# Performance work log

Hardware: AMD Instinct MI355X
Metric: run time of the kernel (lower is better)

The kernel has to match this reference:

```python
import jax, jax.numpy as jnp
import numpy as np
from functools import partial

INPUT_DIM = 256
HIDDEN = 512
NUM_LAYERS = 2

def _linp(key, fan_in, shape):
    # torch nn.Linear/Conv default init: U(-1/sqrt(fan_in), 1/sqrt(fan_in))
    bound = 1.0 / np.sqrt(fan_in)
    return jax.random.uniform(key, shape, jnp.float32, -bound, bound)

def setup_inputs() -> dict:
    key = jax.random.key(0)
    ks = iter(jax.random.split(key, 64))
    d = {}
    d["x"] = jax.random.normal(next(ks), (32, 16, 1, 64, 64), jnp.float32)
    # encoder convs (OIHW)
    d["conv1_w"] = _linp(next(ks), 1 * 9, (16, 1, 3, 3));   d["conv1_b"] = _linp(next(ks), 1 * 9, (16,))
    d["conv2_w"] = _linp(next(ks), 16 * 9, (32, 16, 3, 3)); d["conv2_b"] = _linp(next(ks), 16 * 9, (32,))
    d["conv3_w"] = _linp(next(ks), 32 * 9, (INPUT_DIM, 32, 3, 3)); d["conv3_b"] = _linp(next(ks), 32 * 9, (INPUT_DIM,))
    # LSTM cells: per layer 4 gate linears (forget, input, cell, output), in = input+hidden
    for j in range(NUM_LAYERS):
        fan = (INPUT_DIM if j == 0 else HIDDEN) + HIDDEN
        for g in ("f", "i", "g", "o"):
            d[f"W{g}{j}"] = _linp(next(ks), fan, (fan, HIDDEN))
            d[f"b{g}{j}"] = _linp(next(ks), fan, (HIDDEN,))
    # classifier
    d["cw1"] = _linp(next(ks), HIDDEN, (HIDDEN, 128)); d["cb1"] = _linp(next(ks), HIDDEN, (128,))
    d["cw2"] = _linp(next(ks), 128, (128, 64));        d["cb2"] = _linp(next(ks), 128, (64,))
    d["cw3"] = _linp(next(ks), 64, (64, 6));           d["cb3"] = _linp(next(ks), 64, (6,))
    return d

def _conv(x, w, b):
    y = jax.lax.conv_general_dilated(x, w, (1, 1), "SAME",
                                     dimension_numbers=("NCHW", "OIHW", "NCHW"))
    return y + b[None, :, None, None]

def _maxpool2(x):
    return jax.lax.reduce_window(x, -jnp.inf, jax.lax.max,
                                 (1, 1, 2, 2), (1, 1, 2, 2), "VALID")

def reference(x, conv1_w, conv1_b, conv2_w, conv2_b, conv3_w, conv3_b,
              Wf0, bf0, Wi0, bi0, Wg0, bg0, Wo0, bo0,
              Wf1, bf1, Wi1, bi1, Wg1, bg1, Wo1, bo1,
              cw1, cb1, cw2, cb2, cw3, cb3):
    B, T, C, H, W = x.shape
    xf = x.reshape(B * T, C, H, W)
    h = _maxpool2(jax.nn.relu(_conv(xf, conv1_w, conv1_b)))
    h = _maxpool2(jax.nn.relu(_conv(h, conv2_w, conv2_b)))
    h = jax.nn.relu(_conv(h, conv3_w, conv3_b))
    emb = h.mean(axis=(2, 3)).reshape(B, T, -1)  # AdaptiveAvgPool2d((1,1)); dropout = identity (eval)

    layers = [(Wf0, bf0, Wi0, bi0, Wg0, bg0, Wo0, bo0),
              (Wf1, bf1, Wi1, bi1, Wg1, bg1, Wo1, bo1)]

    def step(carry, x_t):
        hs, cs = carry
        inp = x_t
        new_h, new_c = [], []
        for j, (Wf, bf, Wi, bi, Wg, bg, Wo, bo) in enumerate(layers):
            comb = jnp.concatenate([inp, hs[j]], axis=1)  # [B, in+H]
            f_t = jax.nn.sigmoid(comb @ Wf + bf)
            i_t = jax.nn.sigmoid(comb @ Wi + bi)
            g_t = jnp.tanh(comb @ Wg + bg)
            o_t = jax.nn.sigmoid(comb @ Wo + bo)
            c_n = f_t * cs[j] + i_t * g_t
            h_n = o_t * jnp.tanh(c_n)
            new_h.append(h_n); new_c.append(c_n)
            inp = h_n
        return (tuple(new_h), tuple(new_c)), None

    h0 = tuple(jnp.zeros((B, HIDDEN), x.dtype) for _ in range(NUM_LAYERS))
    c0 = tuple(jnp.zeros((B, HIDDEN), x.dtype) for _ in range(NUM_LAYERS))
    (hs, _), _ = jax.lax.scan(step, (h0, c0), jnp.swapaxes(emb, 0, 1))
    last = hs[-1]  # [B, HIDDEN], last timestep top-layer h (dropout = identity)

    y = jax.nn.relu(last @ cw1 + cb1)
    y = jax.nn.relu(y @ cw2 + cb2)
    return y @ cw3 + cb3  # [B, 6]
```

## Files before the change

### kernel.cpp

```cpp
#include <hip/hip_runtime.h>
#include <math.h>

__global__ void k_conv1(const float* __restrict__ x, const float* __restrict__ w,
                        const float* __restrict__ bias, float* __restrict__ out) {
  int idx = blockIdx.x * 256 + threadIdx.x;
  int ox = idx & 31, oy = (idx >> 5) & 31, oc = (idx >> 10) & 15, n = idx >> 14;
  const float* im = x + n * 4096;
  float wv[9];
#pragma unroll
  for (int i = 0; i < 9; ++i) wv[i] = w[oc * 9 + i];
  float bs = bias[oc];
  float m = 0.f;
#pragma unroll
  for (int dy = 0; dy < 2; ++dy)
#pragma unroll
    for (int dx = 0; dx < 2; ++dx) {
      int cy = oy * 2 + dy, cx = ox * 2 + dx;
      float s = bs;
#pragma unroll
      for (int ky = 0; ky < 3; ++ky) {
        int yy = cy + ky - 1;
        if (yy < 0 || yy >= 64) continue;
#pragma unroll
        for (int kx = 0; kx < 3; ++kx) {
          int xx = cx + kx - 1;
          if (xx < 0 || xx >= 64) continue;
          s += im[yy * 64 + xx] * wv[ky * 3 + kx];
        }
      }
      m = fmaxf(m, fmaxf(s, 0.f));
    }
  out[idx] = m;
}

__global__ void k_prep_w(const float* __restrict__ w2, float* __restrict__ w2t,
                         const float* __restrict__ w3, float* __restrict__ w3t) {
  int id = blockIdx.x * 256 + threadIdx.x;
  if (id < 73728) {
    int ct = id >> 8, oc = id & 255;
    int c = ct / 9, tap = ct - 9 * c;
    w3t[id] = w3[(oc * 32 + c) * 9 + tap];
  }
  if (id < 4608) {
    int ct = id >> 5, oc = id & 31;
    int c = ct / 9, tap = ct - 9 * c;
    w2t[id] = w2[(oc * 16 + c) * 9 + tap];
  }
}

__global__ __launch_bounds__(256) void k_conv2(
    const float* __restrict__ a1, const float* __restrict__ w2t,
    const float* __restrict__ bias, float* __restrict__ a2) {
  __shared__ __align__(16) float ins[8 * 1024];
  int n = blockIdx.x, ocg = blockIdx.y;
  int tid = threadIdx.x;
  int py = tid >> 4, px = tid & 15;
  int y0 = 2 * py - 1, x0 = 2 * px - 1;
  float acc[16][4] = {};
  const float* wb = w2t + ocg * 16;
  for (int ph = 0; ph < 2; ++ph) {
    __syncthreads();
    const float4* src = (const float4*)(a1 + n * 16384 + ph * 8192);
    for (int i = tid; i < 2048; i += 256) ((float4*)ins)[i] = src[i];
    __syncthreads();
    for (int c = 0; c < 8; ++c) {
      float wv[4][4];
#pragma unroll
      for (int r = 0; r < 4; ++r) {
        int y = y0 + r;
        bool vy = (y >= 0) && (y < 32);
        int yc = vy ? y : 0;
#pragma unroll
        for (int cc = 0; cc < 4; ++cc) {
          int xx = x0 + cc;
          bool vx = (xx >= 0) && (xx < 32);
          int xc = vx ? xx : 0;
          float t = ins[c * 1024 + yc * 32 + xc];
          wv[r][cc] = (vy && vx) ? t : 0.f;
        }
      }
      int ch = ph * 8 + c;
#pragma unroll
      for (int ky = 0; ky < 3; ++ky)
#pragma unroll
        for (int kx = 0; kx < 3; ++kx) {
          const float* w16 = wb + (ch * 9 + ky * 3 + kx) * 32;
#pragma unroll
          for (int i = 0; i < 4; ++i) {
            float vv = wv[(i >> 1) + ky][(i & 1) + kx];
#pragma unroll
            for (int j = 0; j < 16; ++j) acc[j][i] += vv * w16[j];
          }
        }
    }
  }
  const float* bp = bias + ocg * 16;
  float4 o[4];
#pragma unroll
  for (int j = 0; j < 16; ++j) {
    float m = fmaxf(fmaxf(acc[j][0], acc[j][1]), fmaxf(acc[j][2], acc[j][3]));
    ((float*)o)[j] = fmaxf(m + bp[j], 0.f);
  }
  float4* dst = (float4*)(a2 + (size_t)(n * 256 + tid) * 32 + ocg * 16);
#pragma unroll
  for (int q = 0; q < 4; ++q) dst[q] = o[q];
}

__global__ __launch_bounds__(256) void k_conv3(
    const float* __restrict__ a2, const float* __restrict__ w3t,
    const float* __restrict__ bias, float* __restrict__ comb0) {
  __shared__ __align__(16) float ins[324 * 20];
  int n = blockIdx.x, ocb = blockIdx.y;
  int tid = threadIdx.x;
  for (int i = tid; i < 1620; i += 256) ((float4*)ins)[i] = float4{0.f, 0.f, 0.f, 0.f};
  int wvid = __builtin_amdgcn_readfirstlane(tid >> 6);
  int lane = tid & 63;
  int tr = lane >> 4, tc = lane & 15;
  float acc[4][8] = {};
  const float* wbase = w3t + ocb * 32 + wvid * 8;
  const float4* src = (const float4*)(a2 + (size_t)n * 8192);
  for (int hf = 0; hf < 2; ++hf) {
    __syncthreads();
    for (int i = tid; i < 1024; i += 256) {
      int px = i >> 2, cg = i & 3;
      int p = ((px >> 4) + 1) * 18 + (px & 15) + 1;
      ((float4*)ins)[p * 5 + cg] = src[px * 8 + hf * 4 + cg];
    }
    __syncthreads();
    for (int cg = 0; cg < 4; ++cg) {
      float4 v[6][3];
#pragma unroll
      for (int dr = 0; dr < 6; ++dr)
#pragma unroll
        for (int dc = 0; dc < 3; ++dc)
          v[dr][dc] = ((const float4*)ins)[((4 * tr + dr) * 18 + tc + dc) * 5 + cg];
#pragma unroll
      for (int ky = 0; ky < 3; ++ky)
#pragma unroll
        for (int kx = 0; kx < 3; ++kx)
#pragma unroll
          for (int c = 0; c < 4; ++c) {
            const float* w8 = wbase + (((hf * 4 + cg) * 4 + c) * 9 + ky * 3 + kx) * 256;
#pragma unroll
            for (int i = 0; i < 4; ++i) {
              float vv = ((const float*)&v[i + ky][kx])[c];
#pragma unroll
              for (int j = 0; j < 8; ++j) acc[i][j] += vv * w8[j];
            }
          }
    }
  }
  const float* bp = bias + ocb * 32 + wvid * 8;
  int bb = n >> 4, tt = n & 15;
#pragma unroll
  for (int j = 0; j < 8; ++j) {
    float bj = bp[j];
    float s = 0.f;
#pragma unroll
    for (int i = 0; i < 4; ++i) s += fmaxf(acc[i][j] + bj, 0.f);
#pragma unroll
    for (int off = 32; off; off >>= 1) s += __shfl_down(s, off, 64);
    if (lane == 0) {
      int oc = ocb * 32 + wvid * 8 + j;
      comb0[(size_t)(tt * 768 + oc) * 32 + bb] = s * (1.f / 256.f);
    }
  }
}

__global__ void k_pack(const float* __restrict__ Wf, const float* __restrict__ Wi,
                       const float* __restrict__ Wg, const float* __restrict__ Wo,
                       float* __restrict__ p, int fan) {
  __shared__ float t[4][32][33];
  int k0 = blockIdx.x * 32, h0 = blockIdx.y * 32;
  int tx = threadIdx.x & 31, ty = threadIdx.x >> 5;
  const float* Ws[4] = {Wf, Wi, Wg, Wo};
#pragma unroll
  for (int g = 0; g < 4; ++g)
    for (int r = 0; r < 32; r += 8)
      t[g][ty + r][tx] = Ws[g][(size_t)(k0 + ty + r) * 512 + h0 + tx];
  __syncthreads();
  for (int r = 0; r < 32; r += 8) {
    int hh = ty + r;
    float4 v = {t[0][tx][hh], t[1][tx][hh], t[2][tx][hh], t[3][tx][hh]};
    ((float4*)p)[(size_t)(h0 + hh) * fan + k0 + tx] = v;
  }
}

struct Coop2Args {
  float* comb0; float* comb1;
  const float* p0; const float* p1;
  const float* b00; const float* b01; const float* b02; const float* b03;
  const float* b10; const float* b11; const float* b12; const float* b13;
  int* bar;
};

#define COOP2_LDS_BYTES (31744 * 4)

template <bool DO0, bool DO1>
__device__ __forceinline__ void fused_step(
    int hbase, int tid, int it, const Coop2Args& A,
    const float4* __restrict__ w40, const float4* __restrict__ w41,
    float* __restrict__ gsum0, float* __restrict__ gsum1,
    float* __restrict__ pre,
    float bf, float bi, float bg, float bo, float& creg) {
  const int C0 = 768 * 32, C1 = 1024 * 32;
  const int hs = tid >> 8, kc = (tid >> 3) & 31, bq = tid & 7;
  float4 f0{0,0,0,0}, i0{0,0,0,0}, g0{0,0,0,0}, o0{0,0,0,0};
  float4 f1{0,0,0,0}, i1{0,0,0,0}, g1{0,0,0,0}, o1{0,0,0,0};
  if constexpr (DO1) {
    const float4* a41 = (const float4*)(A.comb1 + (size_t)(it - 1) * C1)
                        + kc * 8 + bq;
#pragma unroll
    for (int kk = 0; kk < 32; ++kk) {
      float4 w = w41[kk * 32];
      float4 a = a41[kk * 256];
      f1.x += w.x*a.x; f1.y += w.x*a.y; f1.z += w.x*a.z; f1.w += w.x*a.w;
      i1.x += w.y*a.x; i1.y += w.y*a.y; i1.z += w.y*a.z; i1.w += w.y*a.w;
      g1.x += w.z*a.x; g1.y += w.z*a.y; g1.z += w.z*a.z; g1.w += w.z*a.w;
      o1.x += w.w*a.x; o1.y += w.w*a.y; o1.z += w.w*a.z; o1.w += w.w*a.w;
    }
  }
  if constexpr (DO0) {
    const float4* a40 = (const float4*)(A.comb0 + (size_t)it * C0)
                        + kc * 8 + bq;
#pragma unroll
    for (int kk = 0; kk < 24; ++kk) {
      float4 w = w40[kk * 32];
      float4 a = a40[kk * 256];
      f0.x += w.x*a.x; f0.y += w.x*a.y; f0.z += w.x*a.z; f0.w += w.x*a.w;
      i0.x += w.y*a.x; i0.y += w.y*a.y; i0.z += w.y*a.z; i0.w += w.y*a.w;
      g0.x += w.z*a.x; g0.y += w.z*a.y; g0.z += w.z*a.z; g0.w += w.z*a.w;
      o0.x += w.w*a.x; o0.y += w.w*a.y; o0.z += w.w*a.z; o0.w += w.w*a.w;
    }
  }
  __syncthreads();
  if constexpr (DO0) {
    const float* accs[4] = {(const float*)&f0, (const float*)&i0,
                            (const float*)&g0, (const float*)&o0};
#pragma unroll
    for (int g = 0; g < 4; ++g)
#pragma unroll
      for (int j = 0; j < 4; ++j)
        gsum0[((hs * 4 + g) * 32 + 4 * bq + j) * 33 + kc] = accs[g][j];
  }
  if constexpr (DO1) {
    const float* accs[4] = {(const float*)&f1, (const float*)&i1,
                            (const float*)&g1, (const float*)&o1};
#pragma unroll
    for (int g = 0; g < 4; ++g)
#pragma unroll
      for (int j = 0; j < 4; ++j)
        gsum1[((hs * 4 + g) * 32 + 4 * bq + j) * 33 + kc] = accs[g][j];
  }
  __syncthreads();
  {
    int l = tid >> 8, idx = tid & 255;
    int hs2 = idx >> 7, g = (idx >> 5) & 3, b = idx & 31;
    if ((DO0 && l == 0) || (DO1 && l == 1)) {
      const float* gs = l ? gsum1 : gsum0;
      int base = ((hs2 * 4 + g) * 32 + b) * 33;
      float s = 0.f;
#pragma unroll
      for (int q = 0; q < 32; ++q) s += gs[base + q];
      pre[l * 256 + (hs2 * 4 + g) * 32 + b] = s;
    }
  }
  __syncthreads();
  if (tid < 128) {
    int l = tid >> 6, hs2 = (tid >> 5) & 1, b = tid & 31;
    if ((DO0 && l == 0) || (DO1 && l == 1)) {
      const float* pr = pre + l * 256;
      float fp = pr[(hs2 * 4 + 0) * 32 + b] + bf;
      float ip = pr[(hs2 * 4 + 1) * 32 + b] + bi;
      float gp = pr[(hs2 * 4 + 2) * 32 + b] + bg;
      float op = pr[(hs2 * 4 + 3) * 32 + b] + bo;
      float ft = 1.f / (1.f + expf(-fp));
      float it_ = 1.f / (1.f + expf(-ip));
      float gt = tanhf(gp);
      float ot = 1.f / (1.f + expf(-op));
      float cn = ft * creg + it_ * gt;
      creg = cn;
      float hn = ot * tanhf(cn);
      int hh = hbase + hs2;
      if (l == 0) {
        float* hA = A.comb0 + (size_t)(it + 1) * C0 + 256 * 32;
        float* hB = A.comb1 + (size_t)it * C1;
        __hip_atomic_store(&hA[hh * 32 + b], hn, __ATOMIC_RELAXED,
                           __HIP_MEMORY_SCOPE_AGENT);
        __hip_atomic_store(&hB[hh * 32 + b], hn, __ATOMIC_RELAXED,
                           __HIP_MEMORY_SCOPE_AGENT);
      } else {
        float* hA = A.comb1 + (size_t)it * C1 + 512 * 32;
        __hip_atomic_store(&hA[hh * 32 + b], hn, __ATOMIC_RELAXED,
                           __HIP_MEMORY_SCOPE_AGENT);
      }
    }
  }
}

__device__ __forceinline__ void coop_barrier(int* bars, int tid, int bid,
                                             int it) {
  __syncthreads();
  if (tid == 0) {
    int* gb = bars + 32 + (bid & 7) * 32;
    int old = __hip_atomic_fetch_add(gb, 1, __ATOMIC_ACQ_REL,
                                     __HIP_MEMORY_SCOPE_AGENT);
    if (old == 32 * (it + 1) - 1)
      __hip_atomic_fetch_add(bars, 1, __ATOMIC_RELEASE,
                             __HIP_MEMORY_SCOPE_AGENT);
    while (__hip_atomic_load(bars, __ATOMIC_RELAXED,
                             __HIP_MEMORY_SCOPE_AGENT) < 8 * (it + 1))
      __builtin_amdgcn_s_sleep(2);
    __builtin_amdgcn_fence(__ATOMIC_ACQUIRE, "agent");
  }
  __syncthreads();
}

__global__ __launch_bounds__(512) void k_lstm_coop2(Coop2Args A) {
  extern __shared__ float smem[];
  float* wl0 = smem;
  float* wl1 = smem + 6144;
  float* gsum0 = smem + 14336;
  float* gsum1 = smem + 22784;
  float* pre = smem + 31232;
  const int tid = threadIdx.x;
  const int hbase = blockIdx.x * 2;
  for (int i = tid; i < 1536; i += 512) {
    int hs = (i >= 768), k = i - hs * 768;
    ((float4*)wl0)[hs * 768 + k] =
        ((const float4*)A.p0)[(size_t)(hbase + hs) * 768 + k];
  }
  for (int i = tid; i < 2048; i += 512) {
    int hs = i >> 10, k = i & 1023;
    ((float4*)wl1)[hs * 1024 + k] =
        ((const float4*)A.p1)[(size_t)(hbase + hs) * 1024 + k];
  }
  float bf = 0, bi = 0, bg = 0, bo = 0, creg = 0.f;
  if (tid < 64) {
    int hh = hbase + (tid >> 5);
    bf = A.b00[hh]; bi = A.b01[hh]; bg = A.b02[hh]; bo = A.b03[hh];
  } else if (tid < 128) {
    int hh = hbase + ((tid >> 5) & 1);
    bf = A.b10[hh]; bi = A.b11[hh]; bg = A.b12[hh]; bo = A.b13[hh];
  }
  __syncthreads();
  const int hs = tid >> 8, kc = (tid >> 3) & 31;
  const float4* w40 = (const float4*)wl0 + (size_t)hs * 768 + kc;
  const float4* w41 = (const float4*)wl1 + (size_t)hs * 1024 + kc;

  fused_step<true, false>(hbase, tid, 0, A, w40, w41, gsum0, gsum1, pre,
                          bf, bi, bg, bo, creg);
  coop_barrier(A.bar, tid, blockIdx.x, 0);
  for (int it = 1; it < 16; ++it) {
    fused_step<true, true>(hbase, tid, it, A, w40, w41, gsum0, gsum1, pre,
                           bf, bi, bg, bo, creg);
    coop_barrier(A.bar, tid, blockIdx.x, it);
  }
  fused_step<false, true>(hbase, tid, 16, A, w40, w41, gsum0, gsum1, pre,
                          bf, bi, bg, bo, creg);
}

struct SArgs {
  const float* comb; const float* pw;
  float* houtA; float* houtB; float* cT;
  const float* bf; const float* bi; const float* bg; const float* bo;
};

template <int FAN>
__device__ __forceinline__ void lstm_sbody(int h, int tid, const SArgs& A,
                                           float* __restrict__ gsum) {
  constexpr int CH = FAN / 8;
  const int wv = __builtin_amdgcn_readfirstlane(tid >> 6);
  const int lane = tid & 63;
  const int ks = lane >> 5, b = lane & 31;
  const int kb = wv * CH;
  const float4* pw4 = (const float4*)A.pw + (size_t)h * FAN + kb;
  const float* ac = A.comb + (size_t)kb * 32 + lane;
  float a0 = 0.f, a1 = 0.f, a2 = 0.f, a3 = 0.f;
#pragma unroll 8
  for (int kk = 0; kk < CH; kk += 2) {
    float4 w0 = pw4[kk];
    float4 w1 = pw4[kk + 1];
    float av = ac[kk * 32];
    a0 += av * (ks ? w1.x : w0.x);
    a1 += av * (ks ? w1.y : w0.y);
    a2 += av * (ks ? w1.z : w0.z);
    a3 += av * (ks ? w1.w : w0.w);
  }
  a0 += __shfl_xor(a0, 32);
  a1 += __shfl_xor(a1, 32);
  a2 += __shfl_xor(a2, 32);
  a3 += __shfl_xor(a3, 32);
  if (lane < 32) {
    gsum[(wv * 4 + 0) * 33 + b] = a0;
    gsum[(wv * 4 + 1) * 33 + b] = a1;
    gsum[(wv * 4 + 2) * 33 + b] = a2;
    gsum[(wv * 4 + 3) * 33 + b] = a3;
  }
  __syncthreads();
  if (tid < 32) {
    float fp = A.bf[h], ip = A.bi[h], gp = A.bg[h], op = A.bo[h];
#pragma unroll
    for (int q = 0; q < 8; ++q) {
      fp += gsum[(q * 4 + 0) * 33 + tid];
      ip += gsum[(q * 4 + 1) * 33 + tid];
      gp += gsum[(q * 4 + 2) * 33 + tid];
      op += gsum[(q * 4 + 3) * 33 + tid];
    }
    float ft = 1.f / (1.f + expf(-fp));
    float it_ = 1.f / (1.f + expf(-ip));
    float gt = tanhf(gp);
    float ot = 1.f / (1.f + expf(-op));
    float cn = ft * A.cT[h * 32 + tid] + it_ * gt;
    A.cT[h * 32 + tid] = cn;
    float hn = ot * tanhf(cn);
    A.houtA[h * 32 + tid] = hn;
    A.houtB[h * 32 + tid] = hn;
  }
}

__global__ __launch_bounds__(512) void k_lstm_s0(SArgs a) {
  __shared__ float gsum[32 * 33];
  lstm_sbody<768>(blockIdx.x, threadIdx.x, a, gsum);
}
__global__ __launch_bounds__(512) void k_lstm_s1(SArgs a) {
  __shared__ float gsum[32 * 33];
  lstm_sbody<1024>(blockIdx.x, threadIdx.x, a, gsum);
}
__global__ __launch_bounds__(512) void k_lstm_spair(SArgs a0, SArgs a1) {
  __shared__ float gsum[32 * 33];
  if (blockIdx.x < 512)
    lstm_sbody<768>(blockIdx.x, threadIdx.x, a0, gsum);
  else
    lstm_sbody<1024>(blockIdx.x - 512, threadIdx.x, a1, gsum);
}

__global__ void k_cls(const float* __restrict__ h1T, const float* __restrict__ cw1,
                      const float* __restrict__ cb1, const float* __restrict__ cw2,
                      const float* __restrict__ cb2, const float* __restrict__ cw3,
                      const float* __restrict__ cb3, float* __restrict__ out) {
  __shared__ float hv[512];
  __shared__ float y1[128];
  __shared__ float y2[64];
  int b = blockIdx.x, tid = threadIdx.x;
  for (int i = tid; i < 512; i += 128) hv[i] = h1T[i * 32 + b];
  __syncthreads();
  float s = cb1[tid];
  for (int k = 0; k < 512; ++k) s += hv[k] * cw1[k * 128 + tid];
  y1[tid] = fmaxf(s, 0.f);
  __syncthreads();
  if (tid < 64) {
    float s2 = cb2[tid];
    for (int k = 0; k < 128; ++k) s2 += y1[k] * cw2[k * 64 + tid];
    y2[tid] = fmaxf(s2, 0.f);
  }
  __syncthreads();
  if (tid < 6) {
    float s3 = cb3[tid];
    for (int k = 0; k < 64; ++k) s3 += y2[k] * cw3[k * 6 + tid];
    out[b * 6 + tid] = s3;
  }
}

extern "C" void kernel_launch(void* const* d_in, const int* in_sizes, int n_in,
                              void* d_out, int out_size, void* d_ws, size_t ws_size,
                              hipStream_t stream) {
  const float* x  = (const float*)d_in[0];
  const float* w1 = (const float*)d_in[1];
  const float* b1 = (const float*)d_in[2];
  const float* w2 = (const float*)d_in[3];
  const float* b2 = (const float*)d_in[4];
  const float* w3 = (const float*)d_in[5];
  const float* b3 = (const float*)d_in[6];
  const float* cw1 = (const float*)d_in[23];
  const float* cb1 = (const float*)d_in[24];
  const float* cw2 = (const float*)d_in[25];
  const float* cb2 = (const float*)d_in[26];
  const float* cw3 = (const float*)d_in[27];
  const float* cb3 = (const float*)d_in[28];

  float* ws = (float*)d_ws;
  float* a1    = ws;
  float* p0    = ws;
  float* p1    = ws + 1572864;
  float* comb0 = ws + 3670016;
  float* comb1 = ws + 4087808;
  float* c0    = ws + 4644864;
  float* c1    = ws + 4661248;
  int*   bar   = (int*)(ws + 4677632);
  float* a2    = ws + 8388608;
  float* w2t   = ws + 12582912;
  float* w3t   = ws + 12587520;
  const int C0 = 768 * 32, C1 = 1024 * 32;

  k_prep_w<<<288, 256, 0, stream>>>(w2, w2t, w3, w3t);
  k_conv1<<<32768, 256, 0, stream>>>(x, w1, b1, a1);
  k_conv2<<<dim3(512, 2), 256, 0, stream>>>(a1, w2t, b2, a2);

  hipMemsetAsync(comb0 + 256 * 32, 0, (size_t)512 * 32 * 4, stream);
  hipMemsetAsync(comb1 + 512 * 32, 0, (size_t)512 * 32 * 4, stream);
  hipMemsetAsync(c0, 0, (size_t)2 * 512 * 32 * 4, stream);
  hipMemsetAsync(bar, 0, 512 * sizeof(int), stream);

  k_conv3<<<dim3(512, 8), 256, 0, stream>>>(a2, w3t, b3, comb0);

  k_pack<<<dim3(24, 16), 256, 0, stream>>>(
      (const float*)d_in[7], (const float*)d_in[9],
      (const float*)d_in[11], (const float*)d_in[13], p0, 768);
  k_pack<<<dim3(32, 16), 256, 0, stream>>>(
      (const float*)d_in[15], (const float*)d_in[17],
      (const float*)d_in[19], (const float*)d_in[21], p1, 1024);

  Coop2Args ca;
  ca.comb0 = comb0; ca.comb1 = comb1;
  ca.p0 = p0; ca.p1 = p1;
  ca.b00 = (const float*)d_in[8];  ca.b01 = (const float*)d_in[10];
  ca.b02 = (const float*)d_in[12]; ca.b03 = (const float*)d_in[14];
  ca.b10 = (const float*)d_in[16]; ca.b11 = (const float*)d_in[18];
  ca.b12 = (const float*)d_in[20]; ca.b13 = (const float*)d_in[22];
  ca.bar = bar;
  void* kargs[] = {&ca};
  hipError_t cerr = hipLaunchCooperativeKernel(
      (void*)k_lstm_coop2, dim3(256), dim3(512), kargs, COOP2_LDS_BYTES, stream);

  if (cerr != hipSuccess) {
    auto L0 = [&](int t) {
      SArgs a;
      a.comb = comb0 + (size_t)t * C0;
      a.pw = p0;
      a.houtA = comb0 + (size_t)(t + 1) * C0 + 256 * 32;
      a.houtB = comb1 + (size_t)t * C1;
      a.cT = c0;
      a.bf = (const float*)d_in[8];  a.bi = (const float*)d_in[10];
      a.bg = (const float*)d_in[12]; a.bo = (const float*)d_in[14];
      return a;
    };
    auto L1 = [&](int t) {
      SArgs a;
      a.comb = comb1 + (size_t)t * C1;
      a.pw = p1;
      a.houtA = comb1 + (size_t)(t + 1) * C1 + 512 * 32;
      a.houtB = a.houtA;
      a.cT = c1;
      a.bf = (const float*)d_in[16]; a.bi = (const float*)d_in[18];
      a.bg = (const float*)d_in[20]; a.bo = (const float*)d_in[22];
      return a;
    };
    k_lstm_s0<<<512, 512, 0, stream>>>(L0(0));
    for (int p = 0; p < 15; ++p)
      k_lstm_spair<<<1024, 512, 0, stream>>>(L0(p + 1), L1(p));
    k_lstm_s1<<<512, 512, 0, stream>>>(L1(15));
  }

  k_cls<<<32, 128, 0, stream>>>(comb1 + (size_t)16 * C1 + 512 * 32,
                                cw1, cb1, cw2, cb2, cw3, cb3, (float*)d_out);
}
```

Measured before the change: 612.0 us.

## Reuse activation loads across both hidden units in LSTM step; halve conv3 LDS footprint

In the cooperative LSTM kernel, each thread now covers both hidden units of its block and splits K in half, so every activation float4 read from global memory feeds two weight vectors instead of one. The per-step reduction moves to a single shared gsum buffer, used sequentially for layer 0 and then layer 1, with a two-half partial sum. The gate math for both layers runs in the first 64 threads. The conv3 kernel now stages input channels in four phases of 8 channels stored as float2, which cuts its LDS use to raise occupancy at the cost of more barriers. The added syncthreads and the 2-block launch bound could add latency or register pressure.

```diff
diff --git a/kernel.cpp b/kernel.cpp
--- a/kernel.cpp
+++ b/kernel.cpp
@@ -109,41 +109,45 @@
 __global__ __launch_bounds__(256) void k_conv3(
     const float* __restrict__ a2, const float* __restrict__ w3t,
     const float* __restrict__ bias, float* __restrict__ comb0) {
-  __shared__ __align__(16) float ins[324 * 20];
+  __shared__ __align__(16) float ins[324 * 10];
+  float2* ins2 = (float2*)ins;
   int n = blockIdx.x, ocb = blockIdx.y;
   int tid = threadIdx.x;
-  for (int i = tid; i < 1620; i += 256) ((float4*)ins)[i] = float4{0.f, 0.f, 0.f, 0.f};
+  for (int i = tid; i < 810; i += 256) ((float4*)ins)[i] = float4{0.f, 0.f, 0.f, 0.f};
   int wvid = __builtin_amdgcn_readfirstlane(tid >> 6);
   int lane = tid & 63;
   int tr = lane >> 4, tc = lane & 15;
   float acc[4][8] = {};
   const float* wbase = w3t + ocb * 32 + wvid * 8;
   const float4* src = (const float4*)(a2 + (size_t)n * 8192);
-  for (int hf = 0; hf < 2; ++hf) {
+  for (int ph = 0; ph < 4; ++ph) {
     __syncthreads();
-    for (int i = tid; i < 1024; i += 256) {
-      int px = i >> 2, cg = i & 3;
+    for (int i = tid; i < 512; i += 256) {
+      int px = i >> 1, cgl = i & 1;
       int p = ((px >> 4) + 1) * 18 + (px & 15) + 1;
-      ((float4*)ins)[p * 5 + cg] = src[px * 8 + hf * 4 + cg];
+      float4 v = src[px * 8 + ph * 2 + cgl];
+      ins2[p * 5 + cgl * 2]     = float2{v.x, v.y};
+      ins2[p * 5 + cgl * 2 + 1] = float2{v.z, v.w};
     }
     __syncthreads();
-    for (int cg = 0; cg < 4; ++cg) {
-      float4 v[6][3];
+    for (int cg2 = 0; cg2 < 4; ++cg2) {
+      float2 v[6][3];
 #pragma unroll
       for (int dr = 0; dr < 6; ++dr)
 #pragma unroll
         for (int dc = 0; dc < 3; ++dc)
-          v[dr][dc] = ((const float4*)ins)[((4 * tr + dr) * 18 + tc + dc) * 5 + cg];
+          v[dr][dc] = ins2[((4 * tr + dr) * 18 + tc + dc) * 5 + cg2];
 #pragma unroll
       for (int ky = 0; ky < 3; ++ky)
 #pragma unroll
         for (int kx = 0; kx < 3; ++kx)
 #pragma unroll
-          for (int c = 0; c < 4; ++c) {
-            const float* w8 = wbase + (((hf * 4 + cg) * 4 + c) * 9 + ky * 3 + kx) * 256;
+          for (int c = 0; c < 2; ++c) {
+            const float* w8 =
+                wbase + ((ph * 8 + cg2 * 2 + c) * 9 + ky * 3 + kx) * 256;
 #pragma unroll
             for (int i = 0; i < 4; ++i) {
-              float vv = ((const float*)&v[i + ky][kx])[c];
+              float vv = c ? v[i + ky][kx].y : v[i + ky][kx].x;
 #pragma unroll
               for (int j = 0; j < 8; ++j) acc[i][j] += vv * w8[j];
             }
@@ -194,106 +198,121 @@
   int* bar;
 };
 
-#define COOP2_LDS_BYTES (31744 * 4)
+#define COOP2_LDS_BYTES (32512 * 4)
+
+#define FMA4(acc, s, a)                                   \
+  acc.x += (s) * (a).x; acc.y += (s) * (a).y;             \
+  acc.z += (s) * (a).z; acc.w += (s) * (a).w;
 
 template <bool DO0, bool DO1>
 __device__ __forceinline__ void fused_step(
     int hbase, int tid, int it, const Coop2Args& A,
     const float4* __restrict__ w40, const float4* __restrict__ w41,
-    float* __restrict__ gsum0, float* __restrict__ gsum1,
-    float* __restrict__ pre,
-    float bf, float bi, float bg, float bo, float& creg) {
+    float* __restrict__ gsum, float* __restrict__ pre0,
+    float* __restrict__ pre1,
+    float bf0, float bi0, float bg0, float bo0,
+    float bf1, float bi1, float bg1, float bo1,
+    float& c0reg, float& c1reg) {
   const int C0 = 768 * 32, C1 = 1024 * 32;
-  const int hs = tid >> 8, kc = (tid >> 3) & 31, bq = tid & 7;
-  float4 f0{0,0,0,0}, i0{0,0,0,0}, g0{0,0,0,0}, o0{0,0,0,0};
-  float4 f1{0,0,0,0}, i1{0,0,0,0}, g1{0,0,0,0}, o1{0,0,0,0};
+  const int kc = tid >> 3, bq = tid & 7;
+  float4 p0f{0,0,0,0}, p0i{0,0,0,0}, p0g{0,0,0,0}, p0o{0,0,0,0};
+  float4 p1f{0,0,0,0}, p1i{0,0,0,0}, p1g{0,0,0,0}, p1o{0,0,0,0};
+  float4 q0f{0,0,0,0}, q0i{0,0,0,0}, q0g{0,0,0,0}, q0o{0,0,0,0};
+  float4 q1f{0,0,0,0}, q1i{0,0,0,0}, q1g{0,0,0,0}, q1o{0,0,0,0};
   if constexpr (DO1) {
     const float4* a41 = (const float4*)(A.comb1 + (size_t)(it - 1) * C1)
                         + kc * 8 + bq;
 #pragma unroll
-    for (int kk = 0; kk < 32; ++kk) {
-      float4 w = w41[kk * 32];
-      float4 a = a41[kk * 256];
-      f1.x += w.x*a.x; f1.y += w.x*a.y; f1.z += w.x*a.z; f1.w += w.x*a.w;
-      i1.x += w.y*a.x; i1.y += w.y*a.y; i1.z += w.y*a.z; i1.w += w.y*a.w;
-      g1.x += w.z*a.x; g1.y += w.z*a.y; g1.z += w.z*a.z; g1.w += w.z*a.w;
-      o1.x += w.w*a.x; o1.y += w.w*a.y; o1.z += w.w*a.z; o1.w += w.w*a.w;
+    for (int kk = 0; kk < 16; ++kk) {
+      float4 a = a41[kk * 512];
+      float4 u = w41[kk * 64];
+      float4 v = w41[1024 + kk * 64];
+      FMA4(q0f, u.x, a) FMA4(q0i, u.y, a) FMA4(q0g, u.z, a) FMA4(q0o, u.w, a)
+      FMA4(q1f, v.x, a) FMA4(q1i, v.y, a) FMA4(q1g, v.z, a) FMA4(q1o, v.w, a)
     }
   }
   if constexpr (DO0) {
     const float4* a40 = (const float4*)(A.comb0 + (size_t)it * C0)
                         + kc * 8 + bq;
 #pragma unroll
-    for (int kk = 0; kk < 24; ++kk) {
-      float4 w = w40[kk * 32];
-      float4 a = a40[kk * 256];
-      f0.x += w.x*a.x; f0.y += w.x*a.y; f0.z += w.x*a.z; f0.w += w.x*a.w;
-      i0.x += w.y*a.x; i0.y += w.y*a.y; i0.z += w.y*a.z; i0.w += w.y*a.w;
-      g0.x += w.z*a.x; g0.y += w.z*a.y; g0.z += w.z*a.z; g0.w += w.z*a.w;
-      o0.x += w.w*a.x; o0.y += w.w*a.y; o0.z += w.w*a.z; o0.w += w.w*a.w;
-    }
-  }
+    for (int kk = 0; kk < 12; ++kk) {
+      float4 a = a40[kk * 512];
+      float4 u = w40[kk * 64];
+      float4 v = w40[768 + kk * 64];
+      FMA4(p0f, u.x, a) FMA4(p0i, u.y, a) FMA4(p0g, u.z, a) FMA4(p0o, u.w, a)
+      FMA4(p1f, v.x, a) FMA4(p1i, v.y, a) FMA4(p1g, v.z, a) FMA4(p1o, v.w, a)
+    }
+  }
+#define GW(hsv, gv, acc) {                                            \
+    float* _r = gsum + (size_t)(((hsv) * 4 + (gv)) * 32 + 4 * bq) * 67 + kc; \
+    _r[0] = acc.x; _r[67] = acc.y; _r[134] = acc.z; _r[201] = acc.w; }
   __syncthreads();
   if constexpr (DO0) {
-    const float* accs[4] = {(const float*)&f0, (const float*)&i0,
-                            (const float*)&g0, (const float*)&o0};
-#pragma unroll
-    for (int g = 0; g < 4; ++g)
-#pragma unroll
-      for (int j = 0; j < 4; ++j)
-        gsum0[((hs * 4 + g) * 32 + 4 * bq + j) * 33 + kc] = accs[g][j];
-  }
+    GW(0, 0, p0f) GW(0, 1, p0i) GW(0, 2, p0g) GW(0, 3, p0o)
+    GW(1, 0, p1f) GW(1, 1, p1i) GW(1, 2, p1g) GW(1, 3, p1o)
+  }
+  __syncthreads();
+  if constexpr (DO0) {
+    int row = tid & 255, half = tid >> 8;
+    const float* gp = gsum + (size_t)row * 67 + half * 32;
+    float s = 0.f;
+#pragma unroll
+    for (int q = 0; q < 32; ++q) s += gp[q];
+    pre0[half * 256 + row] = s;
+  }
+  __syncthreads();
   if constexpr (DO1) {
-    const float* accs[4] = {(const float*)&f1, (const float*)&i1,
-                            (const float*)&g1, (const float*)&o1};
-#pragma unroll
-    for (int g = 0; g < 4; ++g)
-#pragma unroll
-      for (int j = 0; j < 4; ++j)
-        gsum1[((hs * 4 + g) * 32 + 4 * bq + j) * 33 + kc] = accs[g][j];
-  }
-  __syncthreads();
-  {
-    int l = tid >> 8, idx = tid & 255;
-    int hs2 = idx >> 7, g = (idx >> 5) & 3, b = idx & 31;
-    if ((DO0 && l == 0) || (DO1 && l == 1)) {
-      const float* gs = l ? gsum1 : gsum0;
-      int base = ((hs2 * 4 + g) * 32 + b) * 33;
-      float s = 0.f;
-#pragma unroll
-      for (int q = 0; q < 32; ++q) s += gs[base + q];
-      pre[l * 256 + (hs2 * 4 + g) * 32 + b] = s;
-    }
-  }
-  __syncthreads();
-  if (tid < 128) {
-    int l = tid >> 6, hs2 = (tid >> 5) & 1, b = tid & 31;
-    if ((DO0 && l == 0) || (DO1 && l == 1)) {
-      const float* pr = pre + l * 256;
-      float fp = pr[(hs2 * 4 + 0) * 32 + b] + bf;
-      float ip = pr[(hs2 * 4 + 1) * 32 + b] + bi;
-      float gp = pr[(hs2 * 4 + 2) * 32 + b] + bg;
-      float op = pr[(hs2 * 4 + 3) * 32 + b] + bo;
+    GW(0, 0, q0f) GW(0, 1, q0i) GW(0, 2, q0g) GW(0, 3, q0o)
+    GW(1, 0, q1f) GW(1, 1, q1i) GW(1, 2, q1g) GW(1, 3, q1o)
+  }
+  __syncthreads();
+  if constexpr (DO1) {
+    int row = tid & 255, half = tid >> 8;
+    const float* gp = gsum + (size_t)row * 67 + half * 32;
+    float s = 0.f;
+#pragma unroll
+    for (int q = 0; q < 32; ++q) s += gp[q];
+    pre1[half * 256 + row] = s;
+  }
+  __syncthreads();
+#undef GW
+  if (tid < 64) {
+    int hs2 = tid >> 5, b = tid & 31, hh = hbase + hs2;
+    int r = hs2 * 128 + b;
+    if constexpr (DO0) {
+      float fp = pre0[r] + pre0[256 + r] + bf0;
+      float ip = pre0[r + 32] + pre0[256 + r + 32] + bi0;
+      float gp = pre0[r + 64] + pre0[256 + r + 64] + bg0;
+      float op = pre0[r + 96] + pre0[256 + r + 96] + bo0;
       float ft = 1.f / (1.f + expf(-fp));
       float it_ = 1.f / (1.f + expf(-ip));
       float gt = tanhf(gp);
       float ot = 1.f / (1.f + expf(-op));
-      float cn = ft * creg + it_ * gt;
-      creg = cn;
+      float cn = ft * c0reg + it_ * gt;
+      c0reg = cn;
       float hn = ot * tanhf(cn);
-      int hh = hbase + hs2;
-      if (l == 0) {
-        float* hA = A.comb0 + (size_t)(it + 1) * C0 + 256 * 32;
-        float* hB = A.comb1 + (size_t)it * C1;
-        __hip_atomic_store(&hA[hh * 32 + b], hn, __ATOMIC_RELAXED,
-                           __HIP_MEMORY_SCOPE_AGENT);
-        __hip_atomic_store(&hB[hh * 32 + b], hn, __ATOMIC_RELAXED,
-                           __HIP_MEMORY_SCOPE_AGENT);
-      } else {
-        float* hA = A.comb1 + (size_t)it * C1 + 512 * 32;
-        __hip_atomic_store(&hA[hh * 32 + b], hn, __ATOMIC_RELAXED,
-                           __HIP_MEMORY_SCOPE_AGENT);
-      }
+      float* hA = A.comb0 + (size_t)(it + 1) * C0 + 256 * 32;
+      float* hB = A.comb1 + (size_t)it * C1;
+      __hip_atomic_store(&hA[hh * 32 + b], hn, __ATOMIC_RELAXED,
+                         __HIP_MEMORY_SCOPE_AGENT);
+      __hip_atomic_store(&hB[hh * 32 + b], hn, __ATOMIC_RELAXED,
+                         __HIP_MEMORY_SCOPE_AGENT);
+    }
+    if constexpr (DO1) {
+      float fp = pre1[r] + pre1[256 + r] + bf1;
+      float ip = pre1[r + 32] + pre1[256 + r + 32] + bi1;
+      float gp = pre1[r + 64] + pre1[256 + r + 64] + bg1;
+      float op = pre1[r + 96] + pre1[256 + r + 96] + bo1;
+      float ft = 1.f / (1.f + expf(-fp));
+      float it_ = 1.f / (1.f + expf(-ip));
+      float gt = tanhf(gp);
+      float ot = 1.f / (1.f + expf(-op));
+      float cn = ft * c1reg + it_ * gt;
+      c1reg = cn;
+      float hn = ot * tanhf(cn);
+      float* hA = A.comb1 + (size_t)it * C1 + 512 * 32;
+      __hip_atomic_store(&hA[hh * 32 + b], hn, __ATOMIC_RELAXED,
+                         __HIP_MEMORY_SCOPE_AGENT);
     }
   }
 }
@@ -316,13 +335,13 @@
   __syncthreads();
 }
 
-__global__ __launch_bounds__(512) void k_lstm_coop2(Coop2Args A) {
+__global__ __launch_bounds__(512, 2) void k_lstm_coop2(Coop2Args A) {
   extern __shared__ float smem[];
   float* wl0 = smem;
   float* wl1 = smem + 6144;
-  float* gsum0 = smem + 14336;
-  float* gsum1 = smem + 22784;
-  float* pre = smem + 31232;
+  float* gsum = smem + 14336;
+  float* pre0 = smem + 31488;
+  float* pre1 = smem + 32000;
   const int tid = threadIdx.x;
   const int hbase = blockIdx.x * 2;
   for (int i = tid; i < 1536; i += 512) {
@@ -335,29 +354,29 @@
     ((float4*)wl1)[hs * 1024 + k] =
         ((const float4*)A.p1)[(size_t)(hbase + hs) * 1024 + k];
   }
-  float bf = 0, bi = 0, bg = 0, bo = 0, creg = 0.f;
+  float bf0 = 0, bi0 = 0, bg0 = 0, bo0 = 0;
+  float bf1 = 0, bi1 = 0, bg1 = 0, bo1 = 0;
+  float c0reg = 0.f, c1reg = 0.f;
   if (tid < 64) {
     int hh = hbase + (tid >> 5);
-    bf = A.b00[hh]; bi = A.b01[hh]; bg = A.b02[hh]; bo = A.b03[hh];
-  } else if (tid < 128) {
-    int hh = hbase + ((tid >> 5) & 1);
-    bf = A.b10[hh]; bi = A.b11[hh]; bg = A.b12[hh]; bo = A.b13[hh];
-  }
-  __syncthreads();
-  const int hs = tid >> 8, kc = (tid >> 3) & 31;
-  const float4* w40 = (const float4*)wl0 + (size_t)hs * 768 + kc;
-  const float4* w41 = (const float4*)wl1 + (size_t)hs * 1024 + kc;
-
-  fused_step<true, false>(hbase, tid, 0, A, w40, w41, gsum0, gsum1, pre,
-                          bf, bi, bg, bo, creg);
+    bf0 = A.b00[hh]; bi0 = A.b01[hh]; bg0 = A.b02[hh]; bo0 = A.b03[hh];
+    bf1 = A.b10[hh]; bi1 = A.b11[hh]; bg1 = A.b12[hh]; bo1 = A.b13[hh];
+  }
+  __syncthreads();
+  const int kc = tid >> 3;
+  const float4* w40 = (const float4*)wl0 + kc;
+  const float4* w41 = (const float4*)wl1 + kc;
+
+  fused_step<true, false>(hbase, tid, 0, A, w40, w41, gsum, pre0, pre1,
+                          bf0, bi0, bg0, bo0, bf1, bi1, bg1, bo1, c0reg, c1reg);
   coop_barrier(A.bar, tid, blockIdx.x, 0);
   for (int it = 1; it < 16; ++it) {
-    fused_step<true, true>(hbase, tid, it, A, w40, w41, gsum0, gsum1, pre,
-                           bf, bi, bg, bo, creg);
+    fused_step<true, true>(hbase, tid, it, A, w40, w41, gsum, pre0, pre1,
+                           bf0, bi0, bg0, bo0, bf1, bi1, bg1, bo1, c0reg, c1reg);
     coop_barrier(A.bar, tid, blockIdx.x, it);
   }
-  fused_step<false, true>(hbase, tid, 16, A, w40, w41, gsum0, gsum1, pre,
-                          bf, bi, bg, bo, creg);
+  fused_step<false, true>(hbase, tid, 16, A, w40, w41, gsum, pre0, pre1,
+                          bf0, bi0, bg0, bo0, bf1, bi1, bg1, bo1, c0reg, c1reg);
 }
 
 struct SArgs {
```

Measured after the change: 604.7 us (median of 2 runs). Within noise of the previous version (-1.2%).
